# Kernel tuning notes

Hardware: AMD Instinct MI355X
Metric: run time of the kernel (lower is better)

Reference implementation:

```python
import jax, jax.numpy as jnp
import numpy as np

PARTS = (0.0, 0.25, 0.5, 0.75, 1.0)
N = 16777216


def setup_inputs() -> dict:
    key = jax.random.key(0)
    kx, ky, kd = jax.random.split(key, 3)
    x = jax.random.normal(kx, (N, 2), dtype=jnp.float32)
    y = jax.random.normal(ky, (N, 2), dtype=jnp.float32)
    dist = jax.random.uniform(kd, (N,), dtype=jnp.float32)
    return {"x": x, "y": y, "dist": dist}


def _complex_abs(v):
    # fastmri.complex_abs: sqrt(re^2 + im^2) over last dim of size 2
    return jnp.sqrt(jnp.sum(v * v, axis=-1))


def reference(x, y, dist):
    # Per-element squared errors computed once, then masked-reduced per radial bin.
    diff2_sum = jnp.sum((x - y) ** 2, axis=-1)        # [N] sum over the 2 components
    abs_diff2 = (_complex_abs(x) - _complex_abs(y)) ** 2  # [N]

    loss = jnp.float32(0.0)
    for i in range(len(PARTS) - 1):
        r0, r1 = PARTS[i], PARTS[i + 1]
        mask = (dist >= r0) & (dist <= r1)            # inclusive both ends, as in torch code
        cnt = jnp.sum(mask)                           # number of selected points
        # mse over x[ind] of shape [cnt, 2] -> divide by 2*cnt elements
        mse = jnp.sum(jnp.where(mask, diff2_sum, 0.0)) / jnp.maximum(2 * cnt, 1)
        mse_abs = jnp.sum(jnp.where(mask, abs_diff2, 0.0)) / jnp.maximum(cnt, 1)
        loss = loss + jnp.where(cnt > 0, mse + 0.1 * mse_abs, 0.0)
    return loss
```

## Files before the change

kernel.cpp:

```cpp
#include <hip/hip_runtime.h>

#define NBINS 4
#define BLOCK 256
#define WAVES_PER_BLOCK (BLOCK / 64)
#define NBLOCKS 2048

typedef float f32x4 __attribute__((ext_vector_type(4)));
typedef float f32x2 __attribute__((ext_vector_type(2)));

struct WS {
    float sum_v[NBINS];
    float cnt[NBINS];
};

__device__ __forceinline__ void accum_point(float x0, float x1, float y0, float y1,
                                            float d,
                                            float (&acc)[NBINS], float (&cnt)[NBINS]) {
    float sx = fmaf(x1, x1, x0 * x0);
    float sy = fmaf(y1, y1, y0 * y0);
    float dx0 = x0 - y0, dx1 = x1 - y1;
    float d2 = fmaf(dx1, dx1, dx0 * dx0);
    float t = __builtin_amdgcn_sqrtf(sx * sy);
    float ad2 = sx + sy - 2.0f * t;
    float v = fmaf(0.1f, ad2, 0.5f * d2);
    bool c1 = d < 0.25f;
    bool c2 = d < 0.5f;
    bool c3 = d < 0.75f;
    float m0 = c1 ? 1.0f : 0.0f;
    float m1 = (c2 && !c1) ? 1.0f : 0.0f;
    float m2 = (c3 && !c2) ? 1.0f : 0.0f;
    float m3 = c3 ? 0.0f : 1.0f;
    acc[0] = fmaf(v, m0, acc[0]);
    acc[1] = fmaf(v, m1, acc[1]);
    acc[2] = fmaf(v, m2, acc[2]);
    acc[3] = fmaf(v, m3, acc[3]);
    cnt[0] += m0;
    cnt[1] += m1;
    cnt[2] += m2;
    cnt[3] += m3;
}

__device__ __forceinline__ void accum2v(const f32x4 xv, const f32x4 yv,
                                        const f32x2 dv,
                                        float (&acc)[NBINS], float (&cnt)[NBINS]) {
    accum_point(xv.x, xv.y, yv.x, yv.y, dv.x, acc, cnt);
    accum_point(xv.z, xv.w, yv.z, yv.w, dv.y, acc, cnt);
}

__device__ __forceinline__ f32x4 ntload4(const f32x4* p) {
    return __builtin_nontemporal_load(p);
}
__device__ __forceinline__ f32x2 ntload2(const f32x2* p) {
    return __builtin_nontemporal_load(p);
}

__global__ __launch_bounds__(BLOCK, 4) void radial_loss_main(
    const float* __restrict__ x, const float* __restrict__ y,
    const float* __restrict__ dist, WS* __restrict__ ws, int n) {
    float acc[NBINS] = {0.f, 0.f, 0.f, 0.f};
    float cnt[NBINS] = {0.f, 0.f, 0.f, 0.f};

    const int n2 = n >> 1;
    const f32x4* __restrict__ x4 = (const f32x4*)x;
    const f32x4* __restrict__ y4 = (const f32x4*)y;
    const f32x2* __restrict__ dd = (const f32x2*)dist;

    const int stride = NBLOCKS * BLOCK;
    const int nfull = n2 / stride;
    int i = blockIdx.x * BLOCK + threadIdx.x;

    f32x4 xa, ya, xb, yb;
    f32x2 da, db;
    if (nfull >= 1) { xa = ntload4(x4 + i); ya = ntload4(y4 + i); da = ntload2(dd + i); }
    if (nfull >= 2) {
        xb = ntload4(x4 + i + stride);
        yb = ntload4(y4 + i + stride);
        db = ntload2(dd + i + stride);
    }
#pragma unroll 2
    for (int k = 0; k + 2 < nfull; ++k) {
        f32x4 xc = ntload4(x4 + i + 2 * stride);
        f32x4 yc = ntload4(y4 + i + 2 * stride);
        f32x2 dc = ntload2(dd + i + 2 * stride);
        accum2v(xa, ya, da, acc, cnt);
        xa = xb; ya = yb; da = db;
        xb = xc; yb = yc; db = dc;
        i += stride;
    }
    if (nfull >= 2) {
        accum2v(xa, ya, da, acc, cnt);
        xa = xb; ya = yb; da = db;
        i += stride;
    }
    if (nfull >= 1) {
        accum2v(xa, ya, da, acc, cnt);
        i += stride;
    }
    if (i < n2) {
        accum2v(ntload4(x4 + i), ntload4(y4 + i), ntload2(dd + i), acc, cnt);
    }
    if (blockIdx.x == 0) {
        for (int p = (n2 << 1) + threadIdx.x; p < n; p += BLOCK) {
            accum_point(x[2 * p], x[2 * p + 1], y[2 * p], y[2 * p + 1], dist[p],
                        acc, cnt);
        }
    }

#pragma unroll
    for (int off = 32; off > 0; off >>= 1) {
#pragma unroll
        for (int b = 0; b < NBINS; ++b) {
            acc[b] += __shfl_down(acc[b], off);
            cnt[b] += __shfl_down(cnt[b], off);
        }
    }

    __shared__ float sm_v[WAVES_PER_BLOCK][NBINS];
    __shared__ float sm_c[WAVES_PER_BLOCK][NBINS];
    const int wave = threadIdx.x >> 6;
    const int lane = threadIdx.x & 63;
    if (lane == 0) {
#pragma unroll
        for (int b = 0; b < NBINS; ++b) {
            sm_v[wave][b] = acc[b];
            sm_c[wave][b] = cnt[b];
        }
    }
    __syncthreads();
    if (threadIdx.x < NBINS) {
        const int b = threadIdx.x;
        float tv = 0.f, tc = 0.f;
#pragma unroll
        for (int w = 0; w < WAVES_PER_BLOCK; ++w) {
            tv += sm_v[w][b];
            tc += sm_c[w][b];
        }
        atomicAdd(&ws->sum_v[b], tv);
        atomicAdd(&ws->cnt[b], tc);
    }
}

__global__ void radial_loss_final(const WS* __restrict__ ws, float* __restrict__ out) {
    if (threadIdx.x == 0 && blockIdx.x == 0) {
        float loss = 0.f;
#pragma unroll
        for (int b = 0; b < NBINS; ++b) {
            float c = ws->cnt[b];
            if (c > 0.f) loss += ws->sum_v[b] / c;
        }
        out[0] = loss;
    }
}

extern "C" void kernel_launch(void* const* d_in, const int* in_sizes, int n_in,
                              void* d_out, int out_size, void* d_ws, size_t ws_size,
                              hipStream_t stream) {
    const float* x = (const float*)d_in[0];
    const float* y = (const float*)d_in[1];
    const float* dist = (const float*)d_in[2];
    float* out = (float*)d_out;
    WS* ws = (WS*)d_ws;
    const int n = in_sizes[2];

    hipMemsetAsync(ws, 0, sizeof(WS), stream);
    radial_loss_main<<<NBLOCKS, BLOCK, 0, stream>>>(x, y, dist, ws, n);
    radial_loss_final<<<1, 64, 0, stream>>>(ws, out);
}
```

Measured before the change: 314.8 us.

## Use inline-asm nontemporal loads with manual vmcnt waits for 4-deep prefetch

Replaces the compiler-scheduled two-stage prefetch with a four-stage software pipeline built from inline-asm global_load instructions and explicit s_waitcnt vmcnt counters plus sched barriers. The goal is to keep more memory requests in flight per thread so this bandwidth-bound reduction stays closer to peak HBM throughput. The cost is more live vector registers and fragile hand-written wait counts; the old path is kept as a fallback for other sizes.

```diff
diff --git a/kernel.cpp b/kernel.cpp
--- a/kernel.cpp
+++ b/kernel.cpp
@@ -47,6 +47,16 @@
     accum_point(xv.z, xv.w, yv.z, yv.w, dv.y, acc, cnt);
 }
 
+#define GLOAD4NT(dst, base, off) \
+    asm volatile("global_load_dwordx4 %0, %1, %2 nt" : "=v"(dst) : "v"(off), "s"(base))
+#define GLOAD2NT(dst, base, off) \
+    asm volatile("global_load_dwordx2 %0, %1, %2 nt" : "=v"(dst) : "v"(off), "s"(base))
+#define VWAIT(n)                                              \
+    do {                                                      \
+        asm volatile("s_waitcnt vmcnt(" #n ")" ::: "memory"); \
+        __builtin_amdgcn_sched_barrier(0);                    \
+    } while (0)
+
 __device__ __forceinline__ f32x4 ntload4(const f32x4* p) {
     return __builtin_nontemporal_load(p);
 }
@@ -61,42 +71,75 @@
     float cnt[NBINS] = {0.f, 0.f, 0.f, 0.f};
 
     const int n2 = n >> 1;
-    const f32x4* __restrict__ x4 = (const f32x4*)x;
-    const f32x4* __restrict__ y4 = (const f32x4*)y;
-    const f32x2* __restrict__ dd = (const f32x2*)dist;
-
     const int stride = NBLOCKS * BLOCK;
     const int nfull = n2 / stride;
     int i = blockIdx.x * BLOCK + threadIdx.x;
 
-    f32x4 xa, ya, xb, yb;
-    f32x2 da, db;
-    if (nfull >= 1) { xa = ntload4(x4 + i); ya = ntload4(y4 + i); da = ntload2(dd + i); }
-    if (nfull >= 2) {
-        xb = ntload4(x4 + i + stride);
-        yb = ntload4(y4 + i + stride);
-        db = ntload2(dd + i + stride);
-    }
-#pragma unroll 2
-    for (int k = 0; k + 2 < nfull; ++k) {
-        f32x4 xc = ntload4(x4 + i + 2 * stride);
-        f32x4 yc = ntload4(y4 + i + 2 * stride);
-        f32x2 dc = ntload2(dd + i + 2 * stride);
-        accum2v(xa, ya, da, acc, cnt);
-        xa = xb; ya = yb; da = db;
-        xb = xc; yb = yc; db = dc;
-        i += stride;
-    }
-    if (nfull >= 2) {
-        accum2v(xa, ya, da, acc, cnt);
-        xa = xb; ya = yb; da = db;
-        i += stride;
-    }
-    if (nfull >= 1) {
-        accum2v(xa, ya, da, acc, cnt);
-        i += stride;
-    }
+    if (nfull >= 8 && (nfull & 3) == 0) {
+        f32x4 x0, y0, x1, y1, x2, y2, x3, y3;
+        f32x2 d0, d1, d2, d3;
+#define ISSUE(j, idx)                                       \
+    do {                                                    \
+        unsigned o16 = (unsigned)(idx) * 16u;               \
+        unsigned o8 = (unsigned)(idx) * 8u;                 \
+        GLOAD4NT(x##j, x, o16);                             \
+        GLOAD4NT(y##j, y, o16);                             \
+        GLOAD2NT(d##j, dist, o8);                           \
+    } while (0)
+        ISSUE(0, i);
+        ISSUE(1, i + stride);
+        ISSUE(2, i + 2 * stride);
+        ISSUE(3, i + 3 * stride);
+        int k = 0;
+        for (; k + 8 <= nfull; k += 4) {
+            VWAIT(9); accum2v(x0, y0, d0, acc, cnt); ISSUE(0, i + 4 * stride);
+            VWAIT(9); accum2v(x1, y1, d1, acc, cnt); ISSUE(1, i + 5 * stride);
+            VWAIT(9); accum2v(x2, y2, d2, acc, cnt); ISSUE(2, i + 6 * stride);
+            VWAIT(9); accum2v(x3, y3, d3, acc, cnt); ISSUE(3, i + 7 * stride);
+            i += 4 * stride;
+        }
+        VWAIT(9); accum2v(x0, y0, d0, acc, cnt);
+        VWAIT(6); accum2v(x1, y1, d1, acc, cnt);
+        VWAIT(3); accum2v(x2, y2, d2, acc, cnt);
+        VWAIT(0); accum2v(x3, y3, d3, acc, cnt);
+        i += 4 * stride;
+#undef ISSUE
+    } else {
+        const f32x4* x4 = (const f32x4*)x;
+        const f32x4* y4 = (const f32x4*)y;
+        const f32x2* dd = (const f32x2*)dist;
+        f32x4 xa, ya, xb, yb;
+        f32x2 da, db;
+        if (nfull >= 1) { xa = ntload4(x4 + i); ya = ntload4(y4 + i); da = ntload2(dd + i); }
+        if (nfull >= 2) {
+            xb = ntload4(x4 + i + stride);
+            yb = ntload4(y4 + i + stride);
+            db = ntload2(dd + i + stride);
+        }
+        for (int k = 0; k + 2 < nfull; ++k) {
+            f32x4 xc = ntload4(x4 + i + 2 * stride);
+            f32x4 yc = ntload4(y4 + i + 2 * stride);
+            f32x2 dc = ntload2(dd + i + 2 * stride);
+            accum2v(xa, ya, da, acc, cnt);
+            xa = xb; ya = yb; da = db;
+            xb = xc; yb = yc; db = dc;
+            i += stride;
+        }
+        if (nfull >= 2) {
+            accum2v(xa, ya, da, acc, cnt);
+            xa = xb; ya = yb; da = db;
+            i += stride;
+        }
+        if (nfull >= 1) {
+            accum2v(xa, ya, da, acc, cnt);
+            i += stride;
+        }
+    }
+
     if (i < n2) {
+        const f32x4* x4 = (const f32x4*)x;
+        const f32x4* y4 = (const f32x4*)y;
+        const f32x2* dd = (const f32x2*)dist;
         accum2v(ntload4(x4 + i), ntload4(y4 + i), ntload2(dd + i), acc, cnt);
     }
     if (blockIdx.x == 0) {
```

Measured after the change: 314.5 us. No clear change (-0.1%).
